# Performance work log

Hardware: AMD Instinct MI355X
Metric: run time of the kernel (lower is better)

## Reference

```python
import jax, jax.numpy as jnp
import numpy as np

EPS = 1e-12  # F.normalize default eps


def setup_inputs() -> dict:
    key = jax.random.key(0)
    k1, k2, k3, k4 = jax.random.split(key, 4)
    b, c, h, w = 4, 64, 256, 256
    n_class, n = 19, 20
    nc1 = n_class + 1
    content = jax.random.normal(k1, (b, c, h, w), dtype=jnp.float32)
    seg = jax.random.randint(k2, (b, h, w), 0, n_class, dtype=jnp.int32)
    # xavier-normal-ish init for memory params
    key_mem = jax.random.normal(k3, (nc1, c, n), dtype=jnp.float32) * np.sqrt(2.0 / (c + n))
    val_mem = jax.random.normal(k4, (nc1, n, c), dtype=jnp.float32) * np.sqrt(2.0 / (n + c))
    return {"content": content, "seg": seg, "key_mem": key_mem, "val_mem": val_mem}


def reference(content, seg, key_mem, val_mem):
    # content: [b,c,h,w]; seg: [b,h,w] int; key_mem: [K,c,n]; val_mem: [K,n,c], K=n_class+1
    b, c, h, w = content.shape
    K, _, n = key_mem.shape
    p = h * w
    # one-hot class routing (seg shifted by +1 as in original)
    onehot = jax.nn.one_hot(seg.reshape(b, p) + 1, K, dtype=content.dtype)  # [b,p,K]
    # L2-normalize content rows (masked rows in the original are either this
    # normalized vector, for the matching class, or exactly zero)
    cn = content.transpose(0, 2, 3, 1).reshape(b, p, c)
    cn = cn / jnp.maximum(jnp.linalg.norm(cn, axis=-1, keepdims=True), EPS)
    # L2-normalize keys over channel dim (dim=1 of [K,c,n])
    kn = key_mem / jnp.maximum(jnp.linalg.norm(key_mem, axis=1, keepdims=True), EPS)
    # scores for the matching class; non-matching rows are zero -> softmax = uniform 1/n
    scores = jnp.einsum('bpc,kcn->bkpn', cn, kn)         # [b,K,p,n]
    attn = jax.nn.softmax(scores, axis=-1)
    mask = onehot.transpose(0, 2, 1)[..., None]           # [b,K,p,1]
    weight = jnp.where(mask > 0, attn, 1.0 / n)           # [b,K,p,n]
    # bmm with values, then sum over class dim (fused into the einsum)
    out = jnp.einsum('bkpn,knc->bpc', weight, val_mem)    # [b,p,c]
    return out.reshape(b, h, w, c).transpose(0, 3, 1, 2)  # [b,c,h,w]
```

## Files before the change

### kernel.cpp

```cpp
#include <hip/hip_runtime.h>

typedef _Float16 h2 __attribute__((ext_vector_type(2)));
typedef _Float16 h8 __attribute__((ext_vector_type(8)));
typedef float f4 __attribute__((ext_vector_type(4)));
typedef unsigned int uint32;

#define NVAL 20
#define CDIM 64
#define HW   65536
#define NPIX (4*HW)

#define BLK   512
#define NWAVE (BLK/64)
#define MAXTILES 28
#define MAXSLOT  (MAXTILES*64)

#define KN_OFF      0
#define KN_KSTRIDE  2560
#define VAL_OFF     (20*KN_KSTRIDE)
#define VAL_KSTRIDE 4096
#define VAL_CSTRIDE 64

#define ROW_STRIDE 144
#define ROWS_BYTES (BLK*ROW_STRIDE)
#define INV_OFF   ROWS_BYTES
#define PERM_OFF  (INV_OFF + BLK*4)
#define TCLS_OFF  (PERM_OFF + MAXSLOT*2)
#define FLAG_OFF  (TCLS_OFF + MAXTILES*4)
#define CNT_OFF   (FLAG_OFF + MAXTILES*4)
#define LDS_TOTAL (CNT_OFF + 24*4 + 16)

static __device__ __forceinline__ h2 bch2(uint32 u) { return __builtin_bit_cast(h2, u); }
static __device__ __forceinline__ uint32 bcu(h2 v) { return __builtin_bit_cast(uint32, v); }
static __device__ __forceinline__ h8 bch8(uint4 u) { return __builtin_bit_cast(h8, u); }
static __device__ __forceinline__ h2 pkrtz(float a, float b) {
    return __builtin_bit_cast(h2, __builtin_amdgcn_cvt_pkrtz(a, b));
}

__global__ void prep_kernel(const float* __restrict__ key,
                            const float* __restrict__ val,
                            unsigned char* __restrict__ ws) {
    int i = blockIdx.x * 256 + threadIdx.x;
    if (i < 20*CDIM) {
        int k = i >> 6, c = i & 63;
        const float* vb = val + k*NVAL*CDIM + c;
        float v[NVAL];
        float s = 0.f;
        #pragma unroll
        for (int j = 0; j < NVAL; j++) { v[j] = vb[j*CDIM]; s += v[j]; }
        float t = 0.f;
        for (int kk = 0; kk < 20; kk++) {
            const float* vb2 = val + kk*NVAL*CDIM + c;
            #pragma unroll
            for (int j = 0; j < NVAL; j++) t += vb2[j*CDIM];
        }
        float rest = (t - s) * (1.0f/NVAL);
        uint32* row = (uint32*)(ws + VAL_OFF + (size_t)k*VAL_KSTRIDE + c*VAL_CSTRIDE);
        #pragma unroll
        for (int jp = 0; jp < 10; jp++) row[jp] = bcu(pkrtz(v[2*jp], v[2*jp+1]));
        row[10] = bcu(pkrtz(rest, 0.f));
        #pragma unroll
        for (int jp = 11; jp < 16; jp++) row[jp] = 0u;
    } else if (i < 20*CDIM + 20*NVAL) {
        int idx = i - 20*CDIM;
        int k = idx / NVAL, j = idx % NVAL;
        const float* kb = key + k*CDIM*NVAL + j;
        float x[CDIM];
        float ssq = 0.f;
        #pragma unroll
        for (int c = 0; c < CDIM; c++) { x[c] = kb[c*NVAL]; ssq = fmaf(x[c], x[c], ssq); }
        float inv = 1.0f / fmaxf(sqrtf(ssq), 1e-12f);
        uint32* row = (uint32*)(ws + KN_OFF + (size_t)k*KN_KSTRIDE + j*128);
        #pragma unroll
        for (int cp = 0; cp < 32; cp++) row[cp] = bcu(pkrtz(x[2*cp]*inv, x[2*cp+1]*inv));
    }
}

static __device__ __forceinline__ int2 scan20(const int* cnt, int cls) {
    int acc = 0, mb = 0;
    #pragma unroll
    for (int k = 1; k <= 20; k++) {
        if (k == cls) mb = acc;
        acc += (cnt[k] + 63) & ~63;
    }
    return make_int2(mb, acc >> 6);
}

__global__ __launch_bounds__(BLK, 4) void main_kernel(
        const float* __restrict__ content, const int* __restrict__ seg,
        const unsigned char* __restrict__ tabs, float* __restrict__ out) {
    extern __shared__ unsigned char lds[];
    float* invA = (float*)(lds + INV_OFF);
    unsigned short* perm = (unsigned short*)(lds + PERM_OFF);
    int* tcls  = (int*)(lds + TCLS_OFF);
    int* flags = (int*)(lds + FLAG_OFF);
    int* cnt   = (int*)(lds + CNT_OFF);

    const int tid  = threadIdx.x;
    const int bid  = (int)((blockIdx.x & 7) * 64 + (blockIdx.x >> 3));
    const int gp0  = bid * BLK;
    const int b    = gp0 >> 16;
    const int pim0 = gp0 & (HW - 1);
    float* obase = out + (size_t)b * CDIM * HW + pim0;

    if (tid < 24) cnt[tid] = 0;
    if (tid < MAXTILES) flags[tid] = 0;
    for (int i = tid; i < MAXSLOT; i += BLK) perm[i] = 0xFFFFu;
    __syncthreads();

    const int cls = seg[gp0 + tid] + 1;
    const int myrank = atomicAdd(&cnt[cls], 1);

    {
        const float* cptr = content + (size_t)b * CDIM * HW + pim0 + tid;
        uint2* myrow = (uint2*)(lds + tid * ROW_STRIDE);
        float ssq = 0.f;
        #pragma unroll
        for (int q = 0; q < 16; q++) {
            float f0 = cptr[(size_t)(4*q+0) * HW];
            float f1 = cptr[(size_t)(4*q+1) * HW];
            float f2 = cptr[(size_t)(4*q+2) * HW];
            float f3 = cptr[(size_t)(4*q+3) * HW];
            ssq = fmaf(f0,f0,ssq); ssq = fmaf(f1,f1,ssq);
            ssq = fmaf(f2,f2,ssq); ssq = fmaf(f3,f3,ssq);
            uint2 o; o.x = bcu(pkrtz(f0,f1)); o.y = bcu(pkrtz(f2,f3));
            myrow[q] = o;
        }
        invA[tid] = 1.0f / fmaxf(sqrtf(ssq), 1e-12f);
    }
    __syncthreads();

    const int2 s = scan20(cnt, cls);
    const int myslot = s.x + myrank;
    const int mytile = myslot >> 6;
    {
        perm[myslot] = (unsigned short)tid;
        tcls[mytile] = cls;
    }
    __syncthreads();

    const int nt   = s.y;
    const int wave = tid >> 6, lane = tid & 63;
    const int g = lane >> 4, r16 = lane & 15;

    for (int t = wave; t < nt; t += NWAVE) {
        const int u = __builtin_amdgcn_readfirstlane(tcls[t]);

        int rowb[4];
        float invn[4];
        bool mine[4];
        #pragma unroll
        for (int n = 0; n < 4; n++) {
            int v = perm[t*64 + n*16 + r16];
            mine[n] = (v != 0xFFFF);
            int l = mine[n] ? v : 0;
            rowb[n] = l * ROW_STRIDE;
            invn[n] = invA[l];
        }

        const unsigned char* knc = tabs + KN_OFF + (size_t)u * KN_KSTRIDE;
        uint4 a_sc[2][2];
        #pragma unroll
        for (int m = 0; m < 2; m++)
            #pragma unroll
            for (int ks = 0; ks < 2; ks++)
                a_sc[m][ks] = *(const uint4*)(knc + (m*16 + r16)*128 + (ks*32 + g*8)*2);
        uint4 b_sc[4][2];
        #pragma unroll
        for (int n = 0; n < 4; n++)
            #pragma unroll
            for (int ks = 0; ks < 2; ks++)
                b_sc[n][ks] = *(const uint4*)(lds + rowb[n] + (ks*32 + g*8)*2);

        f4 sacc[2][4];
        #pragma unroll
        for (int m = 0; m < 2; m++)
            #pragma unroll
            for (int n = 0; n < 4; n++) sacc[m][n] = (f4){0.f,0.f,0.f,0.f};
        #pragma unroll
        for (int ks = 0; ks < 2; ks++)
            #pragma unroll
            for (int m = 0; m < 2; m++)
                #pragma unroll
                for (int n = 0; n < 4; n++)
                    sacc[m][n] = __builtin_amdgcn_mfma_f32_16x16x32_f16(
                        bch8(a_sc[m][ks]), bch8(b_sc[n][ks]), sacc[m][n], 0, 0, 0);

        uint2 w0[4], w1[4];
        #pragma unroll
        for (int n = 0; n < 4; n++) {
            float e0[4], e1[4];
            #pragma unroll
            for (int r = 0; r < 4; r++) e0[r] = __expf(sacc[0][n][r] * invn[n]);
            float arg1 = (g == 0) ? invn[n] : 0.0f;
            #pragma unroll
            for (int r = 0; r < 4; r++) e1[r] = __expf(sacc[1][n][r] * arg1);
            float sum = e0[0]+e0[1]+e0[2]+e0[3];
            sum += (g == 0) ? (e1[0]+e1[1]+e1[2]+e1[3]) : 0.0f;
            sum += __shfl_xor(sum, 16, 64);
            sum += __shfl_xor(sum, 32, 64);
            float wsc = 1.0f / sum;
            w0[n].x = bcu(pkrtz(e0[0]*wsc, e0[1]*wsc));
            w0[n].y = bcu(pkrtz(e0[2]*wsc, e0[3]*wsc));
            uint2 t1;
            if (g == 0)      { t1.x = bcu(pkrtz(e1[0]*wsc, e1[1]*wsc));
                               t1.y = bcu(pkrtz(e1[2]*wsc, e1[3]*wsc)); }
            else if (g == 1) { t1.x = 0x00003C00u; t1.y = 0u; }
            else             { t1.x = 0u; t1.y = 0u; }
            w1[n] = t1;
        }
        #pragma unroll
        for (int n = 0; n < 4; n++) {
            if (mine[n]) {
                *(uint2*)(lds + rowb[n] + g*8)      = w0[n];
                *(uint2*)(lds + rowb[n] + 32 + g*8) = w1[n];
            }
        }

        uint4 b_pv[4];
        #pragma unroll
        for (int n = 0; n < 4; n++)
            b_pv[n] = *(const uint4*)(lds + rowb[n] + g*16);
        const unsigned char* vc = tabs + VAL_OFF + (size_t)u * VAL_KSTRIDE;
        #pragma unroll
        for (int m = 0; m < 4; m++) {
            uint4 a = *(const uint4*)(vc + (m*16 + r16)*VAL_CSTRIDE + g*16);
            #pragma unroll
            for (int n = 0; n < 4; n++) {
                f4 o = (f4){0.f,0.f,0.f,0.f};
                o = __builtin_amdgcn_mfma_f32_16x16x32_f16(bch8(a), bch8(b_pv[n]), o, 0, 0, 0);
                uint2 ov; ov.x = bcu(pkrtz(o[0], o[1])); ov.y = bcu(pkrtz(o[2], o[3]));
                if (mine[n])
                    *(uint2*)(lds + rowb[n] + m*32 + g*8) = ov;
            }
        }

        __threadfence_block();
        if (lane == 0)
            __hip_atomic_store(&flags[t], 1, __ATOMIC_RELEASE, __HIP_MEMORY_SCOPE_WORKGROUP);
    }

    while (__hip_atomic_load(&flags[mytile], __ATOMIC_ACQUIRE,
                             __HIP_MEMORY_SCOPE_WORKGROUP) == 0) {
        __builtin_amdgcn_s_sleep(1);
    }
    {
        const uint2* r2 = (const uint2*)(lds + tid * ROW_STRIDE);
        float* op = obase + tid;
        #pragma unroll
        for (int q = 0; q < 16; q++) {
            uint2 v = r2[q];
            h2 x = bch2(v.x), y = bch2(v.y);
            op[(size_t)(4*q+0) * HW] = (float)x[0];
            op[(size_t)(4*q+1) * HW] = (float)x[1];
            op[(size_t)(4*q+2) * HW] = (float)y[0];
            op[(size_t)(4*q+3) * HW] = (float)y[1];
        }
    }
}

extern "C" void kernel_launch(void* const* d_in, const int* in_sizes, int n_in,
                              void* d_out, int out_size, void* d_ws, size_t ws_size,
                              hipStream_t stream) {
    const float* content = (const float*)d_in[0];
    const int*   seg     = (const int*)d_in[1];
    const float* key     = (const float*)d_in[2];
    const float* val     = (const float*)d_in[3];
    float* out = (float*)d_out;
    unsigned char* ws = (unsigned char*)d_ws;

    prep_kernel<<<7, 256, 0, stream>>>(key, val, ws);

    (void)hipFuncSetAttribute((const void*)main_kernel,
                              hipFuncAttributeMaxDynamicSharedMemorySize, LDS_TOTAL);
    main_kernel<<<NPIX/BLK, BLK, LDS_TOTAL, stream>>>(content, seg, ws, out);
}
```

Baseline: 42.04 us.

## Gather content directly into MFMA operands, skipping LDS staging

Drops the per-thread coalesced load of content into fp16 LDS rows and the stored inverse norms; instead each wave loads the permuted pixels' channels from global memory straight into MFMA B registers and computes the norm with cross-lane shuffles. This removes an LDS write/read pass and a barrier-protected staging phase. The trade-off is that global loads are now indexed by the class-sorted permutation, so accesses within a wave are scattered rather than contiguous. The output readback also switches to 16-byte LDS reads.

```diff
diff --git a/kernel.cpp b/kernel.cpp
--- a/kernel.cpp
+++ b/kernel.cpp
@@ -23,8 +23,7 @@
 
 #define ROW_STRIDE 144
 #define ROWS_BYTES (BLK*ROW_STRIDE)
-#define INV_OFF   ROWS_BYTES
-#define PERM_OFF  (INV_OFF + BLK*4)
+#define PERM_OFF  ROWS_BYTES
 #define TCLS_OFF  (PERM_OFF + MAXSLOT*2)
 #define FLAG_OFF  (TCLS_OFF + MAXTILES*4)
 #define CNT_OFF   (FLAG_OFF + MAXTILES*4)
@@ -90,7 +89,6 @@
         const float* __restrict__ content, const int* __restrict__ seg,
         const unsigned char* __restrict__ tabs, float* __restrict__ out) {
     extern __shared__ unsigned char lds[];
-    float* invA = (float*)(lds + INV_OFF);
     unsigned short* perm = (unsigned short*)(lds + PERM_OFF);
     int* tcls  = (int*)(lds + TCLS_OFF);
     int* flags = (int*)(lds + FLAG_OFF);
@@ -101,6 +99,7 @@
     const int gp0  = bid * BLK;
     const int b    = gp0 >> 16;
     const int pim0 = gp0 & (HW - 1);
+    const float* cbase = content + (size_t)b * CDIM * HW + pim0;
     float* obase = out + (size_t)b * CDIM * HW + pim0;
 
     if (tid < 24) cnt[tid] = 0;
@@ -110,24 +109,6 @@
 
     const int cls = seg[gp0 + tid] + 1;
     const int myrank = atomicAdd(&cnt[cls], 1);
-
-    {
-        const float* cptr = content + (size_t)b * CDIM * HW + pim0 + tid;
-        uint2* myrow = (uint2*)(lds + tid * ROW_STRIDE);
-        float ssq = 0.f;
-        #pragma unroll
-        for (int q = 0; q < 16; q++) {
-            float f0 = cptr[(size_t)(4*q+0) * HW];
-            float f1 = cptr[(size_t)(4*q+1) * HW];
-            float f2 = cptr[(size_t)(4*q+2) * HW];
-            float f3 = cptr[(size_t)(4*q+3) * HW];
-            ssq = fmaf(f0,f0,ssq); ssq = fmaf(f1,f1,ssq);
-            ssq = fmaf(f2,f2,ssq); ssq = fmaf(f3,f3,ssq);
-            uint2 o; o.x = bcu(pkrtz(f0,f1)); o.y = bcu(pkrtz(f2,f3));
-            myrow[q] = o;
-        }
-        invA[tid] = 1.0f / fmaxf(sqrtf(ssq), 1e-12f);
-    }
     __syncthreads();
 
     const int2 s = scan20(cnt, cls);
@@ -146,16 +127,44 @@
     for (int t = wave; t < nt; t += NWAVE) {
         const int u = __builtin_amdgcn_readfirstlane(tcls[t]);
 
-        int rowb[4];
-        float invn[4];
+        int px[4], rowb[4];
         bool mine[4];
         #pragma unroll
         for (int n = 0; n < 4; n++) {
             int v = perm[t*64 + n*16 + r16];
             mine[n] = (v != 0xFFFF);
-            int l = mine[n] ? v : 0;
-            rowb[n] = l * ROW_STRIDE;
-            invn[n] = invA[l];
+            px[n]  = mine[n] ? v : 0;
+            rowb[n] = px[n] * ROW_STRIDE;
+        }
+
+        uint4 bsc[4][2];
+        float invn[4];
+        #pragma unroll
+        for (int n = 0; n < 4; n++) {
+            const float* cp = cbase + px[n];
+            float ssq = 0.f;
+            #pragma unroll
+            for (int ks = 0; ks < 2; ks++) {
+                float x0 = cp[(size_t)(ks*32 + g*8 + 0) * HW];
+                float x1 = cp[(size_t)(ks*32 + g*8 + 1) * HW];
+                float x2 = cp[(size_t)(ks*32 + g*8 + 2) * HW];
+                float x3 = cp[(size_t)(ks*32 + g*8 + 3) * HW];
+                float x4 = cp[(size_t)(ks*32 + g*8 + 4) * HW];
+                float x5 = cp[(size_t)(ks*32 + g*8 + 5) * HW];
+                float x6 = cp[(size_t)(ks*32 + g*8 + 6) * HW];
+                float x7 = cp[(size_t)(ks*32 + g*8 + 7) * HW];
+                ssq = fmaf(x0,x0,ssq); ssq = fmaf(x1,x1,ssq);
+                ssq = fmaf(x2,x2,ssq); ssq = fmaf(x3,x3,ssq);
+                ssq = fmaf(x4,x4,ssq); ssq = fmaf(x5,x5,ssq);
+                ssq = fmaf(x6,x6,ssq); ssq = fmaf(x7,x7,ssq);
+                uint4 f;
+                f.x = bcu(pkrtz(x0, x1)); f.y = bcu(pkrtz(x2, x3));
+                f.z = bcu(pkrtz(x4, x5)); f.w = bcu(pkrtz(x6, x7));
+                bsc[n][ks] = f;
+            }
+            ssq += __shfl_xor(ssq, 16, 64);
+            ssq += __shfl_xor(ssq, 32, 64);
+            invn[n] = 1.0f / fmaxf(sqrtf(ssq), 1e-12f);
         }
 
         const unsigned char* knc = tabs + KN_OFF + (size_t)u * KN_KSTRIDE;
@@ -165,12 +174,6 @@
             #pragma unroll
             for (int ks = 0; ks < 2; ks++)
                 a_sc[m][ks] = *(const uint4*)(knc + (m*16 + r16)*128 + (ks*32 + g*8)*2);
-        uint4 b_sc[4][2];
-        #pragma unroll
-        for (int n = 0; n < 4; n++)
-            #pragma unroll
-            for (int ks = 0; ks < 2; ks++)
-                b_sc[n][ks] = *(const uint4*)(lds + rowb[n] + (ks*32 + g*8)*2);
 
         f4 sacc[2][4];
         #pragma unroll
@@ -184,7 +187,7 @@
                 #pragma unroll
                 for (int n = 0; n < 4; n++)
                     sacc[m][n] = __builtin_amdgcn_mfma_f32_16x16x32_f16(
-                        bch8(a_sc[m][ks]), bch8(b_sc[n][ks]), sacc[m][n], 0, 0, 0);
+                        bch8(a_sc[m][ks]), bch8(bsc[n][ks]), sacc[m][n], 0, 0, 0);
 
         uint2 w0[4], w1[4];
         #pragma unroll
@@ -245,16 +248,20 @@
         __builtin_amdgcn_s_sleep(1);
     }
     {
-        const uint2* r2 = (const uint2*)(lds + tid * ROW_STRIDE);
+        const uint4* r4 = (const uint4*)(lds + tid * ROW_STRIDE);
         float* op = obase + tid;
         #pragma unroll
-        for (int q = 0; q < 16; q++) {
-            uint2 v = r2[q];
-            h2 x = bch2(v.x), y = bch2(v.y);
-            op[(size_t)(4*q+0) * HW] = (float)x[0];
-            op[(size_t)(4*q+1) * HW] = (float)x[1];
-            op[(size_t)(4*q+2) * HW] = (float)y[0];
-            op[(size_t)(4*q+3) * HW] = (float)y[1];
+        for (int q = 0; q < 8; q++) {
+            uint4 v = r4[q];
+            h2 x = bch2(v.x), y = bch2(v.y), z = bch2(v.z), w = bch2(v.w);
+            op[(size_t)(8*q+0) * HW] = (float)x[0];
+            op[(size_t)(8*q+1) * HW] = (float)x[1];
+            op[(size_t)(8*q+2) * HW] = (float)y[0];
+            op[(size_t)(8*q+3) * HW] = (float)y[1];
+            op[(size_t)(8*q+4) * HW] = (float)z[0];
+            op[(size_t)(8*q+5) * HW] = (float)z[1];
+            op[(size_t)(8*q+6) * HW] = (float)w[0];
+            op[(size_t)(8*q+7) * HW] = (float)w[1];
         }
     }
 }
```

Result: slower. 79.44 us (+88.9%).
